# Optimization experiments

Hardware: AMD Instinct MI355X
Metric: run time of the kernel (lower is better)

The kernel has to match this reference:

```python
import jax, jax.numpy as jnp
import numpy as np

B, C, D, H, W = 2, 128, 16, 64, 64

def setup_inputs() -> dict:
    key = jax.random.key(0)
    x = jax.random.normal(key, (B, C, D, H, W), dtype=jnp.float32)
    gamma = jnp.zeros((1,), dtype=jnp.float32)
    return {"x": x, "gamma": gamma}

def reference(x, gamma):
    b, c, d, h, w = x.shape
    n = d * h * w
    q = x.reshape(b, c, n)                      # proj_query: B x C x N
    # energy = Q @ K^T where K = Q (same tensor, transposed): B x C x C
    energy = jnp.einsum('bcn,bkn->bck', q, q)
    # max-subtraction trick: energy_new = max(energy, -1) - energy, then softmax
    energy_new = jnp.max(energy, axis=-1, keepdims=True) - energy
    attention = jax.nn.softmax(energy_new, axis=-1)  # B x C x C
    out = jnp.einsum('bck,bkn->bcn', attention, q)   # AV
    out = out.reshape(b, c, d, h, w)
    return gamma * out + x
```

## Files before the change

### kernel.cpp

```cpp
#include <hip/hip_runtime.h>
#include <hip/hip_bf16.h>
#include <stdint.h>

#define BB  2
#define CC  128
#define NNN 65536

typedef __bf16 bf16x8 __attribute__((ext_vector_type(8)));
typedef float  f32x16 __attribute__((ext_vector_type(16)));

__device__ __forceinline__ uint16_t f2bf(float f) {
    uint32_t u = __float_as_uint(f);
    u = (u + 0x7fffu + ((u >> 16) & 1u)) >> 16;
    return (uint16_t)u;
}
__device__ __forceinline__ uint32_t pack2(float a, float b) {
    return (uint32_t)f2bf(a) | ((uint32_t)f2bf(b) << 16);
}

#define GCH  256
#define GST  64
#define GPAD 130

__global__ __launch_bounds__(256) void gram_kernel(const float* __restrict__ x,
        float* __restrict__ partial) {
    const int bid = blockIdx.x;
    const int b   = bid >> 8, chunk = bid & 255;
    const int n0  = chunk * GCH;
    const int t   = threadIdx.x;
    const int w = t >> 6, l = t & 63, h = l >> 5, ln = l & 31;

    __shared__ uint4 lds[2][8 * GPAD];

    const float* xb = x + (size_t)b * CC * NNN;
    const int sc = t >> 3;
    const int sg = t & 7;

    f32x16 acc[4];
#pragma unroll
    for (int j = 0; j < 4; ++j)
#pragma unroll
        for (int r = 0; r < 16; ++r) acc[j][r] = 0.0f;

    float4 va[2][4], vb[2][4];
#pragma unroll
    for (int s2 = 0; s2 < 2; ++s2)
#pragma unroll
        for (int p = 0; p < 4; ++p) {
            const float* gp = xb + (size_t)(sc + 32 * p) * NNN + n0 + s2 * GST + sg * 8;
            va[s2][p] = *(const float4*)(gp);
            vb[s2][p] = *(const float4*)(gp + 4);
        }

    for (int st = 0; st < 4; ++st) {
        const int set = st & 1;
#pragma unroll
        for (int p = 0; p < 4; ++p) {
            uint4 u;
            u.x = pack2(va[set][p].x, va[set][p].y);
            u.y = pack2(va[set][p].z, va[set][p].w);
            u.z = pack2(vb[set][p].x, vb[set][p].y);
            u.w = pack2(vb[set][p].z, vb[set][p].w);
            lds[set][sg * GPAD + sc + 32 * p] = u;
        }
        if (st + 2 < 4) {
#pragma unroll
            for (int p = 0; p < 4; ++p) {
                const float* gp = xb + (size_t)(sc + 32 * p) * NNN + n0 + (st + 2) * GST + sg * 8;
                va[set][p] = *(const float4*)(gp);
                vb[set][p] = *(const float4*)(gp + 4);
            }
        }
        __syncthreads();
#pragma unroll
        for (int s = 0; s < 4; ++s) {
            bf16x8 fa = *(const bf16x8*)&lds[set][(2 * s + h) * GPAD + 32 * w + ln];
#pragma unroll
            for (int j = 0; j < 4; ++j) {
                bf16x8 fb = *(const bf16x8*)&lds[set][(2 * s + h) * GPAD + 32 * j + ln];
                acc[j] = __builtin_amdgcn_mfma_f32_32x32x16_bf16(fa, fb, acc[j], 0, 0, 0);
            }
        }
    }

    float* pb = partial + (size_t)bid * (CC * CC);
#pragma unroll
    for (int j = 0; j < 4; ++j)
#pragma unroll
        for (int r = 0; r < 16; ++r) {
            int row = 32 * w + (r & 3) + 8 * (r >> 2) + 4 * h;
            pb[row * CC + 32 * j + ln] = acc[j][r];
        }
}

__global__ __launch_bounds__(256) void reduce_softmax_kernel(
        const float* __restrict__ partial, const float* __restrict__ gamma,
        uint16_t* __restrict__ attw) {
    const int row = blockIdx.x;
    const int b = row >> 7, i = row & 127;
    const int t = threadIdx.x;
    const int j = t & 127, ph = t >> 7;

    const float* base = partial + ((size_t)(b * 256 + ph * 128)) * (CC * CC)
                      + (size_t)i * CC + j;
    float s0=0,s1=0,s2=0,s3=0,s4=0,s5=0,s6=0,s7=0;
    for (int p = 0; p < 128; p += 8) {
        s0 += base[(size_t)(p + 0) * (CC * CC)];
        s1 += base[(size_t)(p + 1) * (CC * CC)];
        s2 += base[(size_t)(p + 2) * (CC * CC)];
        s3 += base[(size_t)(p + 3) * (CC * CC)];
        s4 += base[(size_t)(p + 4) * (CC * CC)];
        s5 += base[(size_t)(p + 5) * (CC * CC)];
        s6 += base[(size_t)(p + 6) * (CC * CC)];
        s7 += base[(size_t)(p + 7) * (CC * CC)];
    }
    const float sp = ((s0 + s1) + (s2 + s3)) + ((s4 + s5) + (s6 + s7));

    __shared__ float red[256];
    __shared__ float m[128];
    red[t] = sp; __syncthreads();
    const float e = red[j] + red[j + 128];

    if (ph == 0) m[j] = e;
    __syncthreads();
    for (int s = 64; s > 0; s >>= 1) {
        if (ph == 0 && j < s) m[j] = fmaxf(m[j], m[j + s]);
        __syncthreads();
    }
    const float M = m[0]; __syncthreads();
    const float v = M - e;
    if (ph == 0) m[j] = v;
    __syncthreads();
    for (int s = 64; s > 0; s >>= 1) {
        if (ph == 0 && j < s) m[j] = fmaxf(m[j], m[j + s]);
        __syncthreads();
    }
    const float m2 = m[0]; __syncthreads();
    const float pexp = __expf(v - m2);
    if (ph == 0) m[j] = pexp;
    __syncthreads();
    for (int s = 64; s > 0; s >>= 1) {
        if (ph == 0 && j < s) m[j] += m[j + s];
        __syncthreads();
    }
    const float sum = m[0];

    if (ph == 0)
        attw[(size_t)row * CC + j] = f2bf(gamma[0] * pexp / sum);
}

#define AVN 256

__global__ __launch_bounds__(256, 2) void av_kernel(const float* __restrict__ x,
        const uint16_t* __restrict__ attw, float* __restrict__ out) {
    const int bid = blockIdx.x;
    const int b   = bid >> 8;
    const int n0  = (bid & 255) * AVN;
    const int t   = threadIdx.x;
    const int w = t >> 6, l = t & 63, h = l >> 5, ln = l & 31;

    __shared__ uint4 xT[16 * 256];

    const float* xb = x + (size_t)b * CC * NNN;

#pragma unroll
    for (int p = 0; p < 4; ++p) {
        const int g2 = 4 * w + p;
        float4 v[8];
#pragma unroll
        for (int j = 0; j < 8; ++j)
            v[j] = *(const float4*)(xb + (size_t)(8 * g2 + j) * NNN + n0 + 4 * l);
#pragma unroll
        for (int i = 0; i < 4; ++i) {
            const float* f = (const float*)v;
            uint4 u;
            u.x = pack2(v[0].x * 0.f + ((const float*)&v[0])[i], ((const float*)&v[1])[i]);
            u.x = pack2(((const float*)&v[0])[i], ((const float*)&v[1])[i]);
            u.y = pack2(((const float*)&v[2])[i], ((const float*)&v[3])[i]);
            u.z = pack2(((const float*)&v[4])[i], ((const float*)&v[5])[i]);
            u.w = pack2(((const float*)&v[6])[i], ((const float*)&v[7])[i]);
            const int n  = 4 * l + i;
            const int nA = n ^ (l & 7);
            xT[g2 * 256 + nA] = u;
            (void)f;
        }
    }

    bf16x8 fa[8];
    {
        const uint16_t* ab = attw + ((size_t)b * CC + 32 * w + ln) * CC + h * 8;
#pragma unroll
        for (int s = 0; s < 8; ++s)
            fa[s] = *(const bf16x8*)(ab + s * 16);
    }
    __syncthreads();

#pragma unroll
    for (int jt = 0; jt < 8; ++jt) {
        const int n  = 32 * jt + ln;
        const int nA = n ^ ((ln >> 2) & 7);

        float xr[16];
#pragma unroll
        for (int r = 0; r < 16; ++r) {
            int row = (r & 3) + 8 * (r >> 2) + 4 * h;
            xr[r] = xb[(size_t)(32 * w + row) * NNN + n0 + n];
        }

        f32x16 acc;
#pragma unroll
        for (int r = 0; r < 16; ++r) acc[r] = 0.0f;
#pragma unroll
        for (int s = 0; s < 8; ++s) {
            bf16x8 fb = *(const bf16x8*)&xT[(2 * s + h) * 256 + nA];
            acc = __builtin_amdgcn_mfma_f32_32x32x16_bf16(fa[s], fb, acc, 0, 0, 0);
        }
#pragma unroll
        for (int r = 0; r < 16; ++r) {
            int row = (r & 3) + 8 * (r >> 2) + 4 * h;
            out[((size_t)b * CC + 32 * w + row) * NNN + n0 + n] = acc[r] + xr[r];
        }
    }
}

extern "C" void kernel_launch(void* const* d_in, const int* in_sizes, int n_in,
                              void* d_out, int out_size, void* d_ws, size_t ws_size,
                              hipStream_t stream) {
    const float* x     = (const float*)d_in[0];
    const float* gamma = (const float*)d_in[1];
    float* out = (float*)d_out;

    float*    partial = (float*)d_ws;
    uint16_t* att     = (uint16_t*)(partial + (size_t)512 * CC * CC);

    gram_kernel<<<BB * (NNN / GCH), 256, 0, stream>>>(x, partial);
    reduce_softmax_kernel<<<BB * CC, 256, 0, stream>>>(partial, gamma, att);
    av_kernel<<<BB * (NNN / AVN), 256, 0, stream>>>(x, att, out);
}
```

Baseline: 150.3 us.

## Fuse gram, softmax and AV stages into one cooperative kernel with grid syncs

Merges the three kernels into one cooperative launch of 512 blocks with dynamic shared memory, separated by grid-wide syncs and thread fences. This removes two kernel launch gaps and lets the AV phase possibly hit x in cache from the gram phase. In exchange it adds an extra __syncthreads per gram stage, grid barrier costs, idle blocks during the softmax phase, and a 64KB dynamic LDS request that may limit occupancy to two blocks per CU, which is what the cooperative launch needs to keep all 512 blocks resident.

```diff
diff --git a/kernel.cpp b/kernel.cpp
--- a/kernel.cpp
+++ b/kernel.cpp
@@ -1,6 +1,9 @@
 #include <hip/hip_runtime.h>
+#include <hip/hip_cooperative_groups.h>
 #include <hip/hip_bf16.h>
 #include <stdint.h>
+
+namespace cg = cooperative_groups;
 
 #define BB  2
 #define CC  128
@@ -21,204 +24,205 @@
 #define GCH  256
 #define GST  64
 #define GPAD 130
-
-__global__ __launch_bounds__(256) void gram_kernel(const float* __restrict__ x,
-        float* __restrict__ partial) {
+#define AVN  256
+
+__global__ __launch_bounds__(256, 2) void fused_kernel(
+        const float* __restrict__ x, float* __restrict__ partial,
+        const float* __restrict__ gamma, uint16_t* __restrict__ attw,
+        float* __restrict__ out) {
+    extern __shared__ char smem[];
+    cg::grid_group grid = cg::this_grid();
+
     const int bid = blockIdx.x;
-    const int b   = bid >> 8, chunk = bid & 255;
-    const int n0  = chunk * GCH;
     const int t   = threadIdx.x;
     const int w = t >> 6, l = t & 63, h = l >> 5, ln = l & 31;
 
-    __shared__ uint4 lds[2][8 * GPAD];
-
-    const float* xb = x + (size_t)b * CC * NNN;
-    const int sc = t >> 3;
-    const int sg = t & 7;
-
-    f32x16 acc[4];
-#pragma unroll
-    for (int j = 0; j < 4; ++j)
-#pragma unroll
-        for (int r = 0; r < 16; ++r) acc[j][r] = 0.0f;
-
-    float4 va[2][4], vb[2][4];
-#pragma unroll
-    for (int s2 = 0; s2 < 2; ++s2)
+    {
+        uint4* lds = (uint4*)smem;
+        const int b = bid >> 8, chunk = bid & 255;
+        const int n0 = chunk * GCH;
+        const float* xb = x + (size_t)b * CC * NNN;
+        const int sc = t >> 3;
+        const int sg = t & 7;
+
+        f32x16 acc[4];
+#pragma unroll
+        for (int j = 0; j < 4; ++j)
+#pragma unroll
+            for (int r = 0; r < 16; ++r) acc[j][r] = 0.0f;
+
+        float4 va[2][4], vb[2][4];
+#pragma unroll
+        for (int s2 = 0; s2 < 2; ++s2)
+#pragma unroll
+            for (int p = 0; p < 4; ++p) {
+                const float* gp = xb + (size_t)(sc + 32 * p) * NNN + n0 + s2 * GST + sg * 8;
+                va[s2][p] = *(const float4*)(gp);
+                vb[s2][p] = *(const float4*)(gp + 4);
+            }
+
+        for (int st = 0; st < 4; ++st) {
+            const int set = st & 1;
+            uint4* ld = lds + set * (8 * GPAD);
+#pragma unroll
+            for (int p = 0; p < 4; ++p) {
+                uint4 u;
+                u.x = pack2(va[set][p].x, va[set][p].y);
+                u.y = pack2(va[set][p].z, va[set][p].w);
+                u.z = pack2(vb[set][p].x, vb[set][p].y);
+                u.w = pack2(vb[set][p].z, vb[set][p].w);
+                ld[sg * GPAD + sc + 32 * p] = u;
+            }
+            if (st + 2 < 4) {
+#pragma unroll
+                for (int p = 0; p < 4; ++p) {
+                    const float* gp = xb + (size_t)(sc + 32 * p) * NNN + n0 + (st + 2) * GST + sg * 8;
+                    va[set][p] = *(const float4*)(gp);
+                    vb[set][p] = *(const float4*)(gp + 4);
+                }
+            }
+            __syncthreads();
+#pragma unroll
+            for (int s = 0; s < 4; ++s) {
+                bf16x8 fa = *(const bf16x8*)&ld[(2 * s + h) * GPAD + 32 * w + ln];
+#pragma unroll
+                for (int j = 0; j < 4; ++j) {
+                    bf16x8 fb = *(const bf16x8*)&ld[(2 * s + h) * GPAD + 32 * j + ln];
+                    acc[j] = __builtin_amdgcn_mfma_f32_32x32x16_bf16(fa, fb, acc[j], 0, 0, 0);
+                }
+            }
+            __syncthreads();
+        }
+
+        float* pb = partial + (size_t)bid * (CC * CC);
+#pragma unroll
+        for (int j = 0; j < 4; ++j)
+#pragma unroll
+            for (int r = 0; r < 16; ++r) {
+                int row = 32 * w + (r & 3) + 8 * (r >> 2) + 4 * h;
+                pb[row * CC + 32 * j + ln] = acc[j][r];
+            }
+    }
+
+    __threadfence();
+    grid.sync();
+
+    if (bid < BB * CC) {
+        const int row = bid;
+        const int b = row >> 7, i = row & 127;
+        const int j = t & 127, ph = t >> 7;
+
+        const float* base = partial + ((size_t)(b * 256 + ph * 128)) * (CC * CC)
+                          + (size_t)i * CC + j;
+        float s0=0,s1=0,s2=0,s3=0,s4=0,s5=0,s6=0,s7=0;
+        for (int p = 0; p < 128; p += 8) {
+            s0 += base[(size_t)(p + 0) * (CC * CC)];
+            s1 += base[(size_t)(p + 1) * (CC * CC)];
+            s2 += base[(size_t)(p + 2) * (CC * CC)];
+            s3 += base[(size_t)(p + 3) * (CC * CC)];
+            s4 += base[(size_t)(p + 4) * (CC * CC)];
+            s5 += base[(size_t)(p + 5) * (CC * CC)];
+            s6 += base[(size_t)(p + 6) * (CC * CC)];
+            s7 += base[(size_t)(p + 7) * (CC * CC)];
+        }
+        const float sp = ((s0 + s1) + (s2 + s3)) + ((s4 + s5) + (s6 + s7));
+
+        float* red = (float*)smem;
+        float* m   = (float*)smem + 256;
+        red[t] = sp; __syncthreads();
+        const float e = red[j] + red[j + 128];
+
+        if (ph == 0) m[j] = e;
+        __syncthreads();
+        for (int s = 64; s > 0; s >>= 1) {
+            if (ph == 0 && j < s) m[j] = fmaxf(m[j], m[j + s]);
+            __syncthreads();
+        }
+        const float M = m[0]; __syncthreads();
+        const float v = M - e;
+        if (ph == 0) m[j] = v;
+        __syncthreads();
+        for (int s = 64; s > 0; s >>= 1) {
+            if (ph == 0 && j < s) m[j] = fmaxf(m[j], m[j + s]);
+            __syncthreads();
+        }
+        const float m2 = m[0]; __syncthreads();
+        const float pexp = __expf(v - m2);
+        if (ph == 0) m[j] = pexp;
+        __syncthreads();
+        for (int s = 64; s > 0; s >>= 1) {
+            if (ph == 0 && j < s) m[j] += m[j + s];
+            __syncthreads();
+        }
+        const float sum = m[0];
+
+        if (ph == 0)
+            attw[(size_t)row * CC + j] = f2bf(gamma[0] * pexp / sum);
+    }
+
+    __threadfence();
+    grid.sync();
+
+    {
+        uint4* xT = (uint4*)smem;
+        const int b  = bid >> 8;
+        const int n0 = (bid & 255) * AVN;
+        const float* xb = x + (size_t)b * CC * NNN;
+
 #pragma unroll
         for (int p = 0; p < 4; ++p) {
-            const float* gp = xb + (size_t)(sc + 32 * p) * NNN + n0 + s2 * GST + sg * 8;
-            va[s2][p] = *(const float4*)(gp);
-            vb[s2][p] = *(const float4*)(gp + 4);
-        }
-
-    for (int st = 0; st < 4; ++st) {
-        const int set = st & 1;
-#pragma unroll
-        for (int p = 0; p < 4; ++p) {
-            uint4 u;
-            u.x = pack2(va[set][p].x, va[set][p].y);
-            u.y = pack2(va[set][p].z, va[set][p].w);
-            u.z = pack2(vb[set][p].x, vb[set][p].y);
-            u.w = pack2(vb[set][p].z, vb[set][p].w);
-            lds[set][sg * GPAD + sc + 32 * p] = u;
-        }
-        if (st + 2 < 4) {
-#pragma unroll
-            for (int p = 0; p < 4; ++p) {
-                const float* gp = xb + (size_t)(sc + 32 * p) * NNN + n0 + (st + 2) * GST + sg * 8;
-                va[set][p] = *(const float4*)(gp);
-                vb[set][p] = *(const float4*)(gp + 4);
-            }
-        }
-        __syncthreads();
-#pragma unroll
-        for (int s = 0; s < 4; ++s) {
-            bf16x8 fa = *(const bf16x8*)&lds[set][(2 * s + h) * GPAD + 32 * w + ln];
-#pragma unroll
-            for (int j = 0; j < 4; ++j) {
-                bf16x8 fb = *(const bf16x8*)&lds[set][(2 * s + h) * GPAD + 32 * j + ln];
-                acc[j] = __builtin_amdgcn_mfma_f32_32x32x16_bf16(fa, fb, acc[j], 0, 0, 0);
-            }
-        }
-    }
-
-    float* pb = partial + (size_t)bid * (CC * CC);
-#pragma unroll
-    for (int j = 0; j < 4; ++j)
-#pragma unroll
-        for (int r = 0; r < 16; ++r) {
-            int row = 32 * w + (r & 3) + 8 * (r >> 2) + 4 * h;
-            pb[row * CC + 32 * j + ln] = acc[j][r];
-        }
-}
-
-__global__ __launch_bounds__(256) void reduce_softmax_kernel(
-        const float* __restrict__ partial, const float* __restrict__ gamma,
-        uint16_t* __restrict__ attw) {
-    const int row = blockIdx.x;
-    const int b = row >> 7, i = row & 127;
-    const int t = threadIdx.x;
-    const int j = t & 127, ph = t >> 7;
-
-    const float* base = partial + ((size_t)(b * 256 + ph * 128)) * (CC * CC)
-                      + (size_t)i * CC + j;
-    float s0=0,s1=0,s2=0,s3=0,s4=0,s5=0,s6=0,s7=0;
-    for (int p = 0; p < 128; p += 8) {
-        s0 += base[(size_t)(p + 0) * (CC * CC)];
-        s1 += base[(size_t)(p + 1) * (CC * CC)];
-        s2 += base[(size_t)(p + 2) * (CC * CC)];
-        s3 += base[(size_t)(p + 3) * (CC * CC)];
-        s4 += base[(size_t)(p + 4) * (CC * CC)];
-        s5 += base[(size_t)(p + 5) * (CC * CC)];
-        s6 += base[(size_t)(p + 6) * (CC * CC)];
-        s7 += base[(size_t)(p + 7) * (CC * CC)];
-    }
-    const float sp = ((s0 + s1) + (s2 + s3)) + ((s4 + s5) + (s6 + s7));
-
-    __shared__ float red[256];
-    __shared__ float m[128];
-    red[t] = sp; __syncthreads();
-    const float e = red[j] + red[j + 128];
-
-    if (ph == 0) m[j] = e;
-    __syncthreads();
-    for (int s = 64; s > 0; s >>= 1) {
-        if (ph == 0 && j < s) m[j] = fmaxf(m[j], m[j + s]);
-        __syncthreads();
-    }
-    const float M = m[0]; __syncthreads();
-    const float v = M - e;
-    if (ph == 0) m[j] = v;
-    __syncthreads();
-    for (int s = 64; s > 0; s >>= 1) {
-        if (ph == 0 && j < s) m[j] = fmaxf(m[j], m[j + s]);
-        __syncthreads();
-    }
-    const float m2 = m[0]; __syncthreads();
-    const float pexp = __expf(v - m2);
-    if (ph == 0) m[j] = pexp;
-    __syncthreads();
-    for (int s = 64; s > 0; s >>= 1) {
-        if (ph == 0 && j < s) m[j] += m[j + s];
-        __syncthreads();
-    }
-    const float sum = m[0];
-
-    if (ph == 0)
-        attw[(size_t)row * CC + j] = f2bf(gamma[0] * pexp / sum);
-}
-
-#define AVN 256
-
-__global__ __launch_bounds__(256, 2) void av_kernel(const float* __restrict__ x,
-        const uint16_t* __restrict__ attw, float* __restrict__ out) {
-    const int bid = blockIdx.x;
-    const int b   = bid >> 8;
-    const int n0  = (bid & 255) * AVN;
-    const int t   = threadIdx.x;
-    const int w = t >> 6, l = t & 63, h = l >> 5, ln = l & 31;
-
-    __shared__ uint4 xT[16 * 256];
-
-    const float* xb = x + (size_t)b * CC * NNN;
-
-#pragma unroll
-    for (int p = 0; p < 4; ++p) {
-        const int g2 = 4 * w + p;
-        float4 v[8];
-#pragma unroll
-        for (int j = 0; j < 8; ++j)
-            v[j] = *(const float4*)(xb + (size_t)(8 * g2 + j) * NNN + n0 + 4 * l);
-#pragma unroll
-        for (int i = 0; i < 4; ++i) {
-            const float* f = (const float*)v;
-            uint4 u;
-            u.x = pack2(v[0].x * 0.f + ((const float*)&v[0])[i], ((const float*)&v[1])[i]);
-            u.x = pack2(((const float*)&v[0])[i], ((const float*)&v[1])[i]);
-            u.y = pack2(((const float*)&v[2])[i], ((const float*)&v[3])[i]);
-            u.z = pack2(((const float*)&v[4])[i], ((const float*)&v[5])[i]);
-            u.w = pack2(((const float*)&v[6])[i], ((const float*)&v[7])[i]);
-            const int n  = 4 * l + i;
-            const int nA = n ^ (l & 7);
-            xT[g2 * 256 + nA] = u;
-            (void)f;
-        }
-    }
-
-    bf16x8 fa[8];
-    {
-        const uint16_t* ab = attw + ((size_t)b * CC + 32 * w + ln) * CC + h * 8;
-#pragma unroll
-        for (int s = 0; s < 8; ++s)
-            fa[s] = *(const bf16x8*)(ab + s * 16);
-    }
-    __syncthreads();
-
-#pragma unroll
-    for (int jt = 0; jt < 8; ++jt) {
-        const int n  = 32 * jt + ln;
-        const int nA = n ^ ((ln >> 2) & 7);
-
-        float xr[16];
-#pragma unroll
-        for (int r = 0; r < 16; ++r) {
-            int row = (r & 3) + 8 * (r >> 2) + 4 * h;
-            xr[r] = xb[(size_t)(32 * w + row) * NNN + n0 + n];
-        }
-
-        f32x16 acc;
-#pragma unroll
-        for (int r = 0; r < 16; ++r) acc[r] = 0.0f;
-#pragma unroll
-        for (int s = 0; s < 8; ++s) {
-            bf16x8 fb = *(const bf16x8*)&xT[(2 * s + h) * 256 + nA];
-            acc = __builtin_amdgcn_mfma_f32_32x32x16_bf16(fa[s], fb, acc, 0, 0, 0);
-        }
-#pragma unroll
-        for (int r = 0; r < 16; ++r) {
-            int row = (r & 3) + 8 * (r >> 2) + 4 * h;
-            out[((size_t)b * CC + 32 * w + row) * NNN + n0 + n] = acc[r] + xr[r];
+            const int g2 = 4 * w + p;
+            float4 v[8];
+#pragma unroll
+            for (int j = 0; j < 8; ++j)
+                v[j] = *(const float4*)(xb + (size_t)(8 * g2 + j) * NNN + n0 + 4 * l);
+#pragma unroll
+            for (int i = 0; i < 4; ++i) {
+                uint4 u;
+                u.x = pack2(((const float*)&v[0])[i], ((const float*)&v[1])[i]);
+                u.y = pack2(((const float*)&v[2])[i], ((const float*)&v[3])[i]);
+                u.z = pack2(((const float*)&v[4])[i], ((const float*)&v[5])[i]);
+                u.w = pack2(((const float*)&v[6])[i], ((const float*)&v[7])[i]);
+                const int n  = 4 * l + i;
+                const int nA = n ^ (l & 7);
+                xT[g2 * 256 + nA] = u;
+            }
+        }
+
+        bf16x8 fa[8];
+        {
+            const uint16_t* ab = attw + ((size_t)b * CC + 32 * w + ln) * CC + h * 8;
+#pragma unroll
+            for (int s = 0; s < 8; ++s)
+                fa[s] = *(const bf16x8*)(ab + s * 16);
+        }
+        __syncthreads();
+
+#pragma unroll
+        for (int jt = 0; jt < 8; ++jt) {
+            const int n  = 32 * jt + ln;
+            const int nA = n ^ ((ln >> 2) & 7);
+
+            float xr[16];
+#pragma unroll
+            for (int r = 0; r < 16; ++r) {
+                int row = (r & 3) + 8 * (r >> 2) + 4 * h;
+                xr[r] = xb[(size_t)(32 * w + row) * NNN + n0 + n];
+            }
+
+            f32x16 acc;
+#pragma unroll
+            for (int r = 0; r < 16; ++r) acc[r] = 0.0f;
+#pragma unroll
+            for (int s = 0; s < 8; ++s) {
+                bf16x8 fb = *(const bf16x8*)&xT[(2 * s + h) * 256 + nA];
+                acc = __builtin_amdgcn_mfma_f32_32x32x16_bf16(fa[s], fb, acc, 0, 0, 0);
+            }
+#pragma unroll
+            for (int r = 0; r < 16; ++r) {
+                int row = (r & 3) + 8 * (r >> 2) + 4 * h;
+                out[((size_t)b * CC + 32 * w + row) * NNN + n0 + n] = acc[r] + xr[r];
+            }
         }
     }
 }
@@ -233,7 +237,8 @@
     float*    partial = (float*)d_ws;
     uint16_t* att     = (uint16_t*)(partial + (size_t)512 * CC * CC);
 
-    gram_kernel<<<BB * (NNN / GCH), 256, 0, stream>>>(x, partial);
-    reduce_softmax_kernel<<<BB * CC, 256, 0, stream>>>(partial, gamma, att);
-    av_kernel<<<BB * (NNN / AVN), 256, 0, stream>>>(x, att, out);
-}
+    void* args[] = { (void*)&x, (void*)&partial, (void*)&gamma,
+                     (void*)&att, (void*)&out };
+    hipLaunchCooperativeKernel((const void*)fused_kernel,
+                               dim3(512), dim3(256), args, 65536, stream);
+}
```

Result: slower. 369.8 us (+146.1%).

## Double block size to 512 threads in gram and AV kernels, splitting MFMA tiles

Applied to the files above, without the earlier changes.

Both the gram and AV kernels now run 8 waves per block instead of 4. Each wave computes half the previous output tile: two column tiles in gram, and half the n range in AV. Global load mapping and LDS staging are reworked to match, with each gram thread loading 16 contiguous floats of one channel. The aim is more waves in flight to hide memory latency. In exchange, each wave does less MFMA work between syncs, duplicates its A-fragment loads, and the launch bounds of 4 blocks per CU may limit registers.

```diff
diff --git a/kernel.cpp b/kernel.cpp
--- a/kernel.cpp
+++ b/kernel.cpp
@@ -22,62 +22,57 @@
 #define GST  64
 #define GPAD 130
 
-__global__ __launch_bounds__(256) void gram_kernel(const float* __restrict__ x,
+__global__ __launch_bounds__(512, 4) void gram_kernel(const float* __restrict__ x,
         float* __restrict__ partial) {
     const int bid = blockIdx.x;
     const int b   = bid >> 8, chunk = bid & 255;
     const int n0  = chunk * GCH;
     const int t   = threadIdx.x;
-    const int w = t >> 6, l = t & 63, h = l >> 5, ln = l & 31;
+    const int w8 = t >> 6, l = t & 63, h = l >> 5, ln = l & 31;
+    const int strip = w8 >> 1, jh = w8 & 1;
 
     __shared__ uint4 lds[2][8 * GPAD];
 
     const float* xb = x + (size_t)b * CC * NNN;
-    const int sc = t >> 3;
-    const int sg = t & 7;
-
-    f32x16 acc[4];
-#pragma unroll
-    for (int j = 0; j < 4; ++j)
+    const int sc = t >> 2;
+    const int sg = t & 3;
+
+    f32x16 acc[2];
+#pragma unroll
+    for (int j = 0; j < 2; ++j)
 #pragma unroll
         for (int r = 0; r < 16; ++r) acc[j][r] = 0.0f;
 
-    float4 va[2][4], vb[2][4];
+    float4 va[2][4];
 #pragma unroll
     for (int s2 = 0; s2 < 2; ++s2)
 #pragma unroll
-        for (int p = 0; p < 4; ++p) {
-            const float* gp = xb + (size_t)(sc + 32 * p) * NNN + n0 + s2 * GST + sg * 8;
-            va[s2][p] = *(const float4*)(gp);
-            vb[s2][p] = *(const float4*)(gp + 4);
-        }
+        for (int p = 0; p < 4; ++p)
+            va[s2][p] = *(const float4*)(xb + (size_t)sc * NNN + n0 + s2 * GST + sg * 16 + 4 * p);
 
     for (int st = 0; st < 4; ++st) {
         const int set = st & 1;
 #pragma unroll
-        for (int p = 0; p < 4; ++p) {
+        for (int q = 0; q < 2; ++q) {
             uint4 u;
-            u.x = pack2(va[set][p].x, va[set][p].y);
-            u.y = pack2(va[set][p].z, va[set][p].w);
-            u.z = pack2(vb[set][p].x, vb[set][p].y);
-            u.w = pack2(vb[set][p].z, vb[set][p].w);
-            lds[set][sg * GPAD + sc + 32 * p] = u;
+            u.x = pack2(va[set][2 * q].x, va[set][2 * q].y);
+            u.y = pack2(va[set][2 * q].z, va[set][2 * q].w);
+            u.z = pack2(va[set][2 * q + 1].x, va[set][2 * q + 1].y);
+            u.w = pack2(va[set][2 * q + 1].z, va[set][2 * q + 1].w);
+            lds[set][(2 * sg + q) * GPAD + sc] = u;
         }
         if (st + 2 < 4) {
 #pragma unroll
-            for (int p = 0; p < 4; ++p) {
-                const float* gp = xb + (size_t)(sc + 32 * p) * NNN + n0 + (st + 2) * GST + sg * 8;
-                va[set][p] = *(const float4*)(gp);
-                vb[set][p] = *(const float4*)(gp + 4);
-            }
+            for (int p = 0; p < 4; ++p)
+                va[set][p] = *(const float4*)(xb + (size_t)sc * NNN + n0 + (st + 2) * GST + sg * 16 + 4 * p);
         }
         __syncthreads();
 #pragma unroll
         for (int s = 0; s < 4; ++s) {
-            bf16x8 fa = *(const bf16x8*)&lds[set][(2 * s + h) * GPAD + 32 * w + ln];
-#pragma unroll
-            for (int j = 0; j < 4; ++j) {
-                bf16x8 fb = *(const bf16x8*)&lds[set][(2 * s + h) * GPAD + 32 * j + ln];
+            bf16x8 fa = *(const bf16x8*)&lds[set][(2 * s + h) * GPAD + 32 * strip + ln];
+#pragma unroll
+            for (int j = 0; j < 2; ++j) {
+                bf16x8 fb = *(const bf16x8*)&lds[set][(2 * s + h) * GPAD + 32 * (2 * jh + j) + ln];
                 acc[j] = __builtin_amdgcn_mfma_f32_32x32x16_bf16(fa, fb, acc[j], 0, 0, 0);
             }
         }
@@ -85,11 +80,11 @@
 
     float* pb = partial + (size_t)bid * (CC * CC);
 #pragma unroll
-    for (int j = 0; j < 4; ++j)
+    for (int j = 0; j < 2; ++j)
 #pragma unroll
         for (int r = 0; r < 16; ++r) {
-            int row = 32 * w + (r & 3) + 8 * (r >> 2) + 4 * h;
-            pb[row * CC + 32 * j + ln] = acc[j][r];
+            int row = 32 * strip + (r & 3) + 8 * (r >> 2) + 4 * h;
+            pb[row * CC + 32 * (2 * jh + j) + ln] = acc[j][r];
         }
 }
 
@@ -151,44 +146,43 @@
 
 #define AVN 256
 
-__global__ __launch_bounds__(256, 2) void av_kernel(const float* __restrict__ x,
+__global__ __launch_bounds__(512, 4) void av_kernel(const float* __restrict__ x,
         const uint16_t* __restrict__ attw, float* __restrict__ out) {
     const int bid = blockIdx.x;
     const int b   = bid >> 8;
     const int n0  = (bid & 255) * AVN;
     const int t   = threadIdx.x;
-    const int w = t >> 6, l = t & 63, h = l >> 5, ln = l & 31;
+    const int w8 = t >> 6, l = t & 63, h = l >> 5, ln = l & 31;
+    const int strip = w8 >> 1, nh = (w8 & 1) * 128;
 
     __shared__ uint4 xT[16 * 256];
 
     const float* xb = x + (size_t)b * CC * NNN;
 
 #pragma unroll
-    for (int p = 0; p < 4; ++p) {
-        const int g2 = 4 * w + p;
+    for (int p = 0; p < 2; ++p) {
+        const int idx = 512 * p + t;
+        const int g2 = idx >> 6, li = idx & 63;
         float4 v[8];
 #pragma unroll
         for (int j = 0; j < 8; ++j)
-            v[j] = *(const float4*)(xb + (size_t)(8 * g2 + j) * NNN + n0 + 4 * l);
+            v[j] = *(const float4*)(xb + (size_t)(8 * g2 + j) * NNN + n0 + 4 * li);
 #pragma unroll
         for (int i = 0; i < 4; ++i) {
-            const float* f = (const float*)v;
             uint4 u;
-            u.x = pack2(v[0].x * 0.f + ((const float*)&v[0])[i], ((const float*)&v[1])[i]);
             u.x = pack2(((const float*)&v[0])[i], ((const float*)&v[1])[i]);
             u.y = pack2(((const float*)&v[2])[i], ((const float*)&v[3])[i]);
             u.z = pack2(((const float*)&v[4])[i], ((const float*)&v[5])[i]);
             u.w = pack2(((const float*)&v[6])[i], ((const float*)&v[7])[i]);
-            const int n  = 4 * l + i;
-            const int nA = n ^ (l & 7);
+            const int n  = 4 * li + i;
+            const int nA = n ^ (li & 7);
             xT[g2 * 256 + nA] = u;
-            (void)f;
         }
     }
 
     bf16x8 fa[8];
     {
-        const uint16_t* ab = attw + ((size_t)b * CC + 32 * w + ln) * CC + h * 8;
+        const uint16_t* ab = attw + ((size_t)b * CC + 32 * strip + ln) * CC + h * 8;
 #pragma unroll
         for (int s = 0; s < 8; ++s)
             fa[s] = *(const bf16x8*)(ab + s * 16);
@@ -196,15 +190,15 @@
     __syncthreads();
 
 #pragma unroll
-    for (int jt = 0; jt < 8; ++jt) {
-        const int n  = 32 * jt + ln;
+    for (int jt = 0; jt < 4; ++jt) {
+        const int n  = nh + 32 * jt + ln;
         const int nA = n ^ ((ln >> 2) & 7);
 
         float xr[16];
 #pragma unroll
         for (int r = 0; r < 16; ++r) {
             int row = (r & 3) + 8 * (r >> 2) + 4 * h;
-            xr[r] = xb[(size_t)(32 * w + row) * NNN + n0 + n];
+            xr[r] = xb[(size_t)(32 * strip + row) * NNN + n0 + n];
         }
 
         f32x16 acc;
@@ -218,7 +212,7 @@
 #pragma unroll
         for (int r = 0; r < 16; ++r) {
             int row = (r & 3) + 8 * (r >> 2) + 4 * h;
-            out[((size_t)b * CC + 32 * w + row) * NNN + n0 + n] = acc[r] + xr[r];
+            out[((size_t)b * CC + 32 * strip + row) * NNN + n0 + n] = acc[r] + xr[r];
         }
     }
 }
@@ -233,7 +227,7 @@
     float*    partial = (float*)d_ws;
     uint16_t* att     = (uint16_t*)(partial + (size_t)512 * CC * CC);
 
-    gram_kernel<<<BB * (NNN / GCH), 256, 0, stream>>>(x, partial);
+    gram_kernel<<<BB * (NNN / GCH), 512, 0, stream>>>(x, partial);
     reduce_softmax_kernel<<<BB * CC, 256, 0, stream>>>(partial, gamma, att);
-    av_kernel<<<BB * (NNN / AVN), 256, 0, stream>>>(x, att, out);
-}
+    av_kernel<<<BB * (NNN / AVN), 512, 0, stream>>>(x, att, out);
+}
```

Result: no change. 147.4 us (-1.9%).
